# Kernel tuning notes

Hardware: AMD Instinct MI355X
Metric: run time of the kernel (lower is better)

The kernel has to match this reference:

```python
import jax, jax.numpy as jnp
import numpy as np

B, S, H = 32, 256, 128
K, C, DSUB, O = 8, 4096, 16, 6  # PQ subspaces, ncentroids=4096, subvector dim, bits/symbol


def setup_inputs() -> dict:
    key = jax.random.key(0)
    ks = jax.random.split(key, 8)
    return {
        "z": jax.random.normal(ks[0], (B, S, 3), jnp.float32),
        "W1": jax.random.normal(ks[1], (3, H), jnp.float32) * 0.3,
        "b1": jax.random.normal(ks[2], (H,), jnp.float32) * 0.1,
        "W2": jax.random.normal(ks[3], (H, H), jnp.float32) * 0.1,
        "b2": jax.random.normal(ks[4], (H,), jnp.float32) * 0.1,
        "centroids": jax.random.normal(ks[5], (K, C, DSUB), jnp.float32),
        "W3": jax.random.normal(ks[6], (H, O), jnp.float32) * 0.1,
        "b3": jax.random.normal(ks[7], (O,), jnp.float32) * 0.1,
    }


def reference(z, W1, b1, W2, b2, centroids, W3, b3):
    # Small demapper MLP (layers 1-2, exact dense math)
    h1 = jax.nn.relu(z @ W1 + b1)            # [B,S,H]
    h2 = jax.nn.relu(h1 @ W2 + b2)           # [B,S,H] == layer3in
    N = B * S
    x = h2.reshape(N, K, DSUB)               # split rows into K PQ subvectors
    # Encode: nearest centroid per subspace (||x-c||^2 argmin; ||x||^2 is constant per row)
    dots = jnp.einsum("nkd,kcd->nkc", x, centroids)      # [N,K,C]
    c_norm = jnp.sum(centroids * centroids, axis=-1)      # [K,C]
    codes = jnp.argmin(c_norm[None, :, :] - 2.0 * dots, axis=-1)  # [N,K] int
    # LUT: precomputed centroid @ W3 per subspace
    W3r = W3.reshape(K, DSUB, O)
    lut = jnp.einsum("kcd,kdo->kco", centroids, W3r)      # [K,C,O]
    # Approximate matmul: sum of LUT entries selected by codes
    approx = jnp.sum(lut[jnp.arange(K)[None, :], codes], axis=1)  # [N,O]
    llr = (approx + b3).reshape(B, S * O)                 # [B, n]
    return llr
```

## Files before the change

kernel.cpp:

```cpp
#include <hip/hip_runtime.h>
#include <hip/hip_fp16.h>
#include <stdint.h>

#define NROWS 8192
#define HDIM  128
#define KSUB  8
#define NC    4096
#define DSUB  16
#define OUTD  6

#define FB_TAU 3e-4f
#define DOTSCALE (-2.0f / 4096.0f)

typedef _Float16 f16x8 __attribute__((ext_vector_type(8)));
typedef float    f32x4 __attribute__((ext_vector_type(4)));

#define XK_OFF 0u
#define CN_OFF 4194304u
#define B1_OFF 4325376u
#define PK_OFF 6422528u

__global__ __launch_bounds__(256) void prep_kernel(
    const float* __restrict__ z, const float* __restrict__ W1, const float* __restrict__ b1,
    const float* __restrict__ W2, const float* __restrict__ b2,
    const float* __restrict__ ce,
    float* __restrict__ xk, float* __restrict__ cnorm, f16x8* __restrict__ B1S)
{
    __shared__ float h1s[32 * HDIM];
    __shared__ float w2s[HDIM * HDIM];
    const int t = threadIdx.x;
    const int row0 = blockIdx.x * 32;

    #pragma unroll
    for (int q = 0; q < 2; ++q) {
        const int e = blockIdx.x * 512 + q * 256 + t;
        const int k    = e >> 14;
        const int tile = (e >> 6) & 255;
        const int lane = e & 63;
        const int col  = lane & 15;
        const int quad = lane >> 4;
        const int dims = (quad & 1) * 8;
        const int part = quad >> 1;
        const int n = tile * 16 + col;
        const float* cp = &ce[((size_t)k * NC + n) * DSUB + dims];
        f16x8 hi, lo;
        #pragma unroll
        for (int j = 0; j < 8; ++j) {
            const float s = cp[j] * 16.0f;
            const _Float16 h = (_Float16)s;
            hi[j] = h;
            lo[j] = (_Float16)(s - (float)h);
        }
        B1S[e] = part ? lo : hi;
    }

    if (blockIdx.x < (KSUB * NC) / 256) {
        const int g = blockIdx.x * 256 + t;
        const float4* cp = (const float4*)&ce[(size_t)g * DSUB];
        float nn = 0.f;
        #pragma unroll
        for (int q = 0; q < 4; ++q) {
            const float4 v = cp[q];
            nn = fmaf(v.x, v.x, nn); nn = fmaf(v.y, v.y, nn);
            nn = fmaf(v.z, v.z, nn); nn = fmaf(v.w, v.w, nn);
        }
        cnorm[g] = nn;
    }

    {
        const float4* g4 = (const float4*)W2;
        float4* s4 = (float4*)w2s;
        #pragma unroll
        for (int q = 0; q < 16; ++q) s4[t + q * 256] = g4[t + q * 256];
    }

    #pragma unroll
    for (int e = 0; e < 16; ++e) {
        const int idx = e * 256 + t;
        const int r = idx >> 7, j = idx & 127;
        const int n = row0 + r;
        float acc = b1[j];
        acc = fmaf(z[n * 3 + 0], W1[0 * HDIM + j], acc);
        acc = fmaf(z[n * 3 + 1], W1[1 * HDIM + j], acc);
        acc = fmaf(z[n * 3 + 2], W1[2 * HDIM + j], acc);
        h1s[idx] = fmaxf(acc, 0.f);
    }
    __syncthreads();

    const int c4 = (t & 31) * 4;
    const int r4 = (t >> 5) * 4;
    float acc[4][4];
    #pragma unroll
    for (int a = 0; a < 4; ++a)
        #pragma unroll
        for (int b = 0; b < 4; ++b) acc[a][b] = 0.f;

    for (int k4 = 0; k4 < HDIM; k4 += 4) {
        float hh[4][4], ww[4][4];
        #pragma unroll
        for (int q = 0; q < 4; ++q) {
            const float4 v = *(const float4*)&h1s[(r4 + q) * HDIM + k4];
            hh[q][0] = v.x; hh[q][1] = v.y; hh[q][2] = v.z; hh[q][3] = v.w;
        }
        #pragma unroll
        for (int p = 0; p < 4; ++p) {
            const float4 v = *(const float4*)&w2s[(k4 + p) * HDIM + c4];
            ww[p][0] = v.x; ww[p][1] = v.y; ww[p][2] = v.z; ww[p][3] = v.w;
        }
        #pragma unroll
        for (int q = 0; q < 4; ++q)
            #pragma unroll
            for (int p = 0; p < 4; ++p) {
                acc[q][0] = fmaf(hh[q][p], ww[p][0], acc[q][0]);
                acc[q][1] = fmaf(hh[q][p], ww[p][1], acc[q][1]);
                acc[q][2] = fmaf(hh[q][p], ww[p][2], acc[q][2]);
                acc[q][3] = fmaf(hh[q][p], ww[p][3], acc[q][3]);
            }
    }

    const float4 bb = *(const float4*)&b2[c4];
    const int kk = c4 >> 4;
    const int dd = c4 & 15;
    #pragma unroll
    for (int q = 0; q < 4; ++q) {
        float4 o;
        o.x = fmaxf(acc[q][0] + bb.x, 0.f);
        o.y = fmaxf(acc[q][1] + bb.y, 0.f);
        o.z = fmaxf(acc[q][2] + bb.z, 0.f);
        o.w = fmaxf(acc[q][3] + bb.w, 0.f);
        *(float4*)&xk[((size_t)kk * NROWS + (row0 + r4 + q)) * DSUB + dd] = o;
    }
}

__global__ __launch_bounds__(256, 4) void argmin_kernel(
    const float* __restrict__ xk, const f16x8* __restrict__ B1S,
    const float* __restrict__ cnorm, unsigned long long* __restrict__ pk)
{
    __shared__ f16x8 cs[16 * 64];
    __shared__ float cnL[1024];
    const int t = threadIdx.x;
    const int lane = t & 63;
    const int wid  = t >> 6;
    const int k  = blockIdx.y;
    const int cz = blockIdx.z;
    const int rb = blockIdx.x * 4 + wid;
    const int col  = lane & 15;
    const int quad = lane >> 4;
    const int dims = (quad & 1) * 8;
    const int part = quad >> 1;

    {
        const float* cnp0 = &cnorm[k * NC + cz * 1024];
        #pragma unroll
        for (int q = 0; q < 4; ++q) cnL[t + q * 256] = cnp0[t + q * 256];
    }

    f16x8 A[2];
    #pragma unroll
    for (int g = 0; g < 2; ++g) {
        const int row = rb * 32 + g * 16 + col;
        const float* xp = &xk[((size_t)k * NROWS + row) * DSUB + dims];
        f16x8 hi, lo;
        #pragma unroll
        for (int j = 0; j < 8; ++j) {
            const float s = xp[j] * 256.0f;
            const _Float16 h = (_Float16)s;
            hi[j] = h;
            lo[j] = (_Float16)(s - (float)h);
        }
        A[g] = part ? lo : hi;
    }

    float m1[2][4], m2[2][4];
    int   idx[2][4];
    #pragma unroll
    for (int g = 0; g < 2; ++g)
        #pragma unroll
        for (int j = 0; j < 4; ++j) { m1[g][j] = 1e30f; m2[g][j] = 1e30f; idx[g][j] = 0; }

    const f16x8* gp = &B1S[((size_t)k * 256 + cz * 64) * 64];

    for (int ch = 0; ch < 4; ++ch) {
        __syncthreads();
        {
            const uint4* g4 = (const uint4*)(gp + (size_t)ch * 1024);
            uint4* s4 = (uint4*)cs;
            #pragma unroll
            for (int q = 0; q < 4; ++q) s4[t + q * 256] = g4[t + q * 256];
        }
        __syncthreads();

        #pragma unroll 2
        for (int tt = 0; tt < 16; ++tt) {
            const f16x8 b1 = cs[tt * 64 + lane];
            const f16x8 b2 = cs[tt * 64 + (lane ^ 32)];
            const float nrm = cnL[(ch * 16 + tt) * 16 + col];
            const f32x4 zz = {0.f, 0.f, 0.f, 0.f};
            f32x4 p0 = __builtin_amdgcn_mfma_f32_16x16x32_f16(A[0], b1, zz, 0, 0, 0);
            p0       = __builtin_amdgcn_mfma_f32_16x16x32_f16(A[0], b2, p0, 0, 0, 0);
            f32x4 p1 = __builtin_amdgcn_mfma_f32_16x16x32_f16(A[1], b1, zz, 0, 0, 0);
            p1       = __builtin_amdgcn_mfma_f32_16x16x32_f16(A[1], b2, p1, 0, 0, 0);
            const int c = ((cz * 64 + ch * 16 + tt) << 4) + col;
            #pragma unroll
            for (int j = 0; j < 4; ++j) {
                {
                    const float s = fmaf(p0[j], DOTSCALE, nrm);
                    const bool lt = s < m1[0][j];
                    m2[0][j] = __builtin_amdgcn_fmed3f(s, m1[0][j], m2[0][j]);
                    idx[0][j] = lt ? c : idx[0][j];
                    m1[0][j] = fminf(s, m1[0][j]);
                }
                {
                    const float s = fmaf(p1[j], DOTSCALE, nrm);
                    const bool lt = s < m1[1][j];
                    m2[1][j] = __builtin_amdgcn_fmed3f(s, m1[1][j], m2[1][j]);
                    idx[1][j] = lt ? c : idx[1][j];
                    m1[1][j] = fminf(s, m1[1][j]);
                }
            }
        }
    }

    #pragma unroll
    for (int off = 1; off < 16; off <<= 1) {
        #pragma unroll
        for (int g = 0; g < 2; ++g)
            #pragma unroll
            for (int j = 0; j < 4; ++j) {
                const float om1 = __shfl_xor(m1[g][j], off, 64);
                const float om2 = __shfl_xor(m2[g][j], off, 64);
                const int  oidx = __shfl_xor(idx[g][j], off, 64);
                const bool better = (om1 < m1[g][j]) ||
                                    (om1 == m1[g][j] && oidx < idx[g][j]);
                m2[g][j] = fminf(fminf(m2[g][j], om2), fmaxf(m1[g][j], om1));
                m1[g][j] = better ? om1 : m1[g][j];
                idx[g][j] = better ? oidx : idx[g][j];
            }
    }

    if (col == 0) {
        #pragma unroll
        for (int g = 0; g < 2; ++g)
            #pragma unroll
            for (int j = 0; j < 4; ++j) {
                const int row = rb * 32 + g * 16 + quad * 4 + j;
                unsigned u = __float_as_uint(m1[g][j]);
                u = (u & 0x80000000u) ? ~u : (u | 0x80000000u);
                const unsigned short dh =
                    __half_as_ushort(__float2half(m2[g][j] - m1[g][j]));
                pk[((size_t)cz * NROWS + row) * KSUB + k] =
                    ((unsigned long long)u << 32) |
                    ((unsigned)dh << 16) | (unsigned)idx[g][j];
            }
    }
}

__global__ __launch_bounds__(256) void finish_kernel(
    const float* __restrict__ xk, const float* __restrict__ ce,
    const float* __restrict__ cnorm, const unsigned long long* __restrict__ pk,
    const float* __restrict__ W3, const float* __restrict__ b3,
    float* __restrict__ out)
{
    __shared__ int codes_s[256];
    __shared__ int wl_s[256];
    __shared__ int wcnt;
    const int t = threadIdx.x;
    const int row0 = blockIdx.x * 32;
    if (t == 0) wcnt = 0;
    __syncthreads();

    {
        const int row = row0 + (t >> 3);
        const int k = t & 7;
        unsigned long long p[4];
        #pragma unroll
        for (int s = 0; s < 4; ++s)
            p[s] = pk[((size_t)s * NROWS + row) * KSUB + k];
        unsigned long long w = p[0];
        #pragma unroll
        for (int s = 1; s < 4; ++s) w = p[s] < w ? p[s] : w;
        const unsigned uw = (unsigned)(w >> 32);
        const float m1w = __uint_as_float((uw & 0x80000000u) ? (uw ^ 0x80000000u) : ~uw);
        float m2g = m1w + (float)__ushort_as_half((unsigned short)((unsigned)w >> 16));
        #pragma unroll
        for (int s = 0; s < 4; ++s) {
            if (p[s] != w) {
                const unsigned us = (unsigned)(p[s] >> 32);
                m2g = fminf(m2g, __uint_as_float(
                    (us & 0x80000000u) ? (us ^ 0x80000000u) : ~us));
            }
        }
        codes_s[t] = (int)(w & 0xFFFFull);
        if (m2g - m1w < FB_TAU) {
            const int slot = atomicAdd(&wcnt, 1);
            wl_s[slot] = t;
        }
    }
    __syncthreads();

    {
        const int lane = t & 63;
        const int wid = t >> 6;
        const int nitems = wcnt;
        for (int i = wid; i < nitems; i += 4) {
            const int wg = wl_s[i];
            const int row = row0 + (wg >> 3), k = wg & 7;
            float xr[DSUB];
            {
                const float* xp = &xk[((size_t)k * NROWS + row) * DSUB];
                #pragma unroll
                for (int q = 0; q < DSUB; q += 4) {
                    const float4 v = *(const float4*)&xp[q];
                    xr[q + 0] = -2.f * v.x; xr[q + 1] = -2.f * v.y;
                    xr[q + 2] = -2.f * v.z; xr[q + 3] = -2.f * v.w;
                }
            }
            float bm = 1e30f; int bi = NC;
            for (int c = lane; c < NC; c += 64) {
                const float* cp = &ce[((size_t)k * NC + c) * DSUB];
                float s = cnorm[k * NC + c];
                #pragma unroll
                for (int d = 0; d < DSUB; ++d) s = fmaf(xr[d], cp[d], s);
                if (s < bm) { bm = s; bi = c; }
            }
            #pragma unroll
            for (int off = 1; off < 64; off <<= 1) {
                const float om = __shfl_xor(bm, off, 64);
                const int  oi = __shfl_xor(bi, off, 64);
                const bool better = (om < bm) || (om == bm && oi < bi);
                bm = better ? om : bm;
                bi = better ? oi : bi;
            }
            if (lane == 0) codes_s[wg] = bi;
        }
    }
    __syncthreads();

    if (t < 32 * OUTD) {
        const int nl = t / OUTD;
        const int o = t - nl * OUTD;
        const int n = row0 + nl;
        float acc = b3[o];
        #pragma unroll
        for (int k = 0; k < KSUB; ++k) {
            const int code = codes_s[nl * KSUB + k];
            const float* cp = &ce[((size_t)k * NC + code) * DSUB];
            const float* wp = &W3[(k * DSUB) * OUTD + o];
            #pragma unroll
            for (int d = 0; d < DSUB; ++d)
                acc = fmaf(cp[d], wp[d * OUTD], acc);
        }
        out[n * OUTD + o] = acc;
    }
}

extern "C" void kernel_launch(void* const* d_in, const int* in_sizes, int n_in,
                              void* d_out, int out_size, void* d_ws, size_t ws_size,
                              hipStream_t stream)
{
    const float* z  = (const float*)d_in[0];
    const float* W1 = (const float*)d_in[1];
    const float* b1 = (const float*)d_in[2];
    const float* W2 = (const float*)d_in[3];
    const float* b2 = (const float*)d_in[4];
    const float* ce = (const float*)d_in[5];
    const float* W3 = (const float*)d_in[6];
    const float* b3 = (const float*)d_in[7];

    char* ws = (char*)d_ws;
    float* xk    = (float*)(ws + XK_OFF);
    float* cnorm = (float*)(ws + CN_OFF);
    f16x8* B1S   = (f16x8*)(ws + B1_OFF);
    unsigned long long* pk = (unsigned long long*)(ws + PK_OFF);

    hipLaunchKernelGGL(prep_kernel, dim3(256), dim3(256), 0, stream,
                       z, W1, b1, W2, b2, ce, xk, cnorm, B1S);
    hipLaunchKernelGGL(argmin_kernel, dim3(64, 8, 4), dim3(256), 0, stream,
                       xk, B1S, cnorm, pk);
    hipLaunchKernelGGL(finish_kernel, dim3(256), dim3(256), 0, stream,
                       xk, ce, cnorm, pk, W3, b3, (float*)d_out);
}
```

Measured before the change: 170.4 us.

## Switch argmin to 32x32x16 MFMA tiles and halve centroid splits

Replaces the 16x16x32 MFMA tiling in the argmin kernel with 32x32x16 MFMA. Each wave handles 32 rows by 32 centroids per step, with the hi/lo fp16 split now carried as four explicit MFMAs. The centroid split dimension drops from 4 to 2, so each block covers 2048 centroids with twice the LDS staging, and finish merges only two partial results. The aim is fewer LDS reads per MFMA and larger outputs per instruction, at the cost of more accumulator registers (16 rows of m1, m2 and idx) and half as many blocks in the grid.

```diff
diff --git a/kernel.cpp b/kernel.cpp
--- a/kernel.cpp
+++ b/kernel.cpp
@@ -13,18 +13,18 @@
 #define DOTSCALE (-2.0f / 4096.0f)
 
 typedef _Float16 f16x8 __attribute__((ext_vector_type(8)));
-typedef float    f32x4 __attribute__((ext_vector_type(4)));
+typedef float    f32x16 __attribute__((ext_vector_type(16)));
 
 #define XK_OFF 0u
 #define CN_OFF 4194304u
-#define B1_OFF 4325376u
+#define B2_OFF 4325376u
 #define PK_OFF 6422528u
 
 __global__ __launch_bounds__(256) void prep_kernel(
     const float* __restrict__ z, const float* __restrict__ W1, const float* __restrict__ b1,
     const float* __restrict__ W2, const float* __restrict__ b2,
     const float* __restrict__ ce,
-    float* __restrict__ xk, float* __restrict__ cnorm, f16x8* __restrict__ B1S)
+    float* __restrict__ xk, float* __restrict__ cnorm, f16x8* __restrict__ B2S)
 {
     __shared__ float h1s[32 * HDIM];
     __shared__ float w2s[HDIM * HDIM];
@@ -35,13 +35,11 @@
     for (int q = 0; q < 2; ++q) {
         const int e = blockIdx.x * 512 + q * 256 + t;
         const int k    = e >> 14;
-        const int tile = (e >> 6) & 255;
+        const int unit = (e >> 7) & 127;
+        const int half = (e >> 6) & 1;
         const int lane = e & 63;
-        const int col  = lane & 15;
-        const int quad = lane >> 4;
-        const int dims = (quad & 1) * 8;
-        const int part = quad >> 1;
-        const int n = tile * 16 + col;
+        const int n    = unit * 32 + (lane & 31);
+        const int dims = (lane >> 5) * 8;
         const float* cp = &ce[((size_t)k * NC + n) * DSUB + dims];
         f16x8 hi, lo;
         #pragma unroll
@@ -51,7 +49,7 @@
             hi[j] = h;
             lo[j] = (_Float16)(s - (float)h);
         }
-        B1S[e] = part ? lo : hi;
+        B2S[e] = half ? lo : hi;
     }
 
     if (blockIdx.x < (KSUB * NC) / 256) {
@@ -133,125 +131,105 @@
 }
 
 __global__ __launch_bounds__(256, 4) void argmin_kernel(
-    const float* __restrict__ xk, const f16x8* __restrict__ B1S,
+    const float* __restrict__ xk, const f16x8* __restrict__ B2S,
     const float* __restrict__ cnorm, unsigned long long* __restrict__ pk)
 {
-    __shared__ f16x8 cs[16 * 64];
-    __shared__ float cnL[1024];
+    __shared__ f16x8 cs[16 * 2 * 64];
+    __shared__ float cnS[2048];
     const int t = threadIdx.x;
     const int lane = t & 63;
     const int wid  = t >> 6;
     const int k  = blockIdx.y;
     const int cz = blockIdx.z;
-    const int rb = blockIdx.x * 4 + wid;
-    const int col  = lane & 15;
-    const int quad = lane >> 4;
-    const int dims = (quad & 1) * 8;
-    const int part = quad >> 1;
-
-    {
-        const float* cnp0 = &cnorm[k * NC + cz * 1024];
-        #pragma unroll
-        for (int q = 0; q < 4; ++q) cnL[t + q * 256] = cnp0[t + q * 256];
-    }
-
-    f16x8 A[2];
-    #pragma unroll
-    for (int g = 0; g < 2; ++g) {
-        const int row = rb * 32 + g * 16 + col;
-        const float* xp = &xk[((size_t)k * NROWS + row) * DSUB + dims];
-        f16x8 hi, lo;
+    const int rowbase = blockIdx.x * 128 + wid * 32;
+    const int col = lane & 31;
+    const int khl = lane >> 5;
+
+    {
+        const float* cnp0 = &cnorm[k * NC + cz * 2048];
+        #pragma unroll
+        for (int q = 0; q < 8; ++q) cnS[t + q * 256] = cnp0[t + q * 256];
+    }
+
+    f16x8 Ah, Al;
+    {
+        const float* xp = &xk[((size_t)k * NROWS + rowbase + col) * DSUB + khl * 8];
         #pragma unroll
         for (int j = 0; j < 8; ++j) {
             const float s = xp[j] * 256.0f;
             const _Float16 h = (_Float16)s;
-            hi[j] = h;
-            lo[j] = (_Float16)(s - (float)h);
-        }
-        A[g] = part ? lo : hi;
-    }
-
-    float m1[2][4], m2[2][4];
-    int   idx[2][4];
-    #pragma unroll
-    for (int g = 0; g < 2; ++g)
-        #pragma unroll
-        for (int j = 0; j < 4; ++j) { m1[g][j] = 1e30f; m2[g][j] = 1e30f; idx[g][j] = 0; }
-
-    const f16x8* gp = &B1S[((size_t)k * 256 + cz * 64) * 64];
+            Ah[j] = h;
+            Al[j] = (_Float16)(s - (float)h);
+        }
+    }
+
+    float m1[16], m2[16];
+    int   idx[16];
+    #pragma unroll
+    for (int r = 0; r < 16; ++r) { m1[r] = 1e30f; m2[r] = 1e30f; idx[r] = 0; }
+
+    const f16x8* gB = &B2S[((size_t)(k * 128 + cz * 64)) * 128];
+    const f32x16 zero16 = {0.f,0.f,0.f,0.f,0.f,0.f,0.f,0.f,
+                           0.f,0.f,0.f,0.f,0.f,0.f,0.f,0.f};
 
     for (int ch = 0; ch < 4; ++ch) {
         __syncthreads();
         {
-            const uint4* g4 = (const uint4*)(gp + (size_t)ch * 1024);
+            const uint4* g4 = (const uint4*)gB + ch * 2048;
             uint4* s4 = (uint4*)cs;
             #pragma unroll
-            for (int q = 0; q < 4; ++q) s4[t + q * 256] = g4[t + q * 256];
+            for (int q = 0; q < 8; ++q) s4[t + q * 256] = g4[t + q * 256];
         }
         __syncthreads();
 
         #pragma unroll 2
-        for (int tt = 0; tt < 16; ++tt) {
-            const f16x8 b1 = cs[tt * 64 + lane];
-            const f16x8 b2 = cs[tt * 64 + (lane ^ 32)];
-            const float nrm = cnL[(ch * 16 + tt) * 16 + col];
-            const f32x4 zz = {0.f, 0.f, 0.f, 0.f};
-            f32x4 p0 = __builtin_amdgcn_mfma_f32_16x16x32_f16(A[0], b1, zz, 0, 0, 0);
-            p0       = __builtin_amdgcn_mfma_f32_16x16x32_f16(A[0], b2, p0, 0, 0, 0);
-            f32x4 p1 = __builtin_amdgcn_mfma_f32_16x16x32_f16(A[1], b1, zz, 0, 0, 0);
-            p1       = __builtin_amdgcn_mfma_f32_16x16x32_f16(A[1], b2, p1, 0, 0, 0);
-            const int c = ((cz * 64 + ch * 16 + tt) << 4) + col;
-            #pragma unroll
-            for (int j = 0; j < 4; ++j) {
-                {
-                    const float s = fmaf(p0[j], DOTSCALE, nrm);
-                    const bool lt = s < m1[0][j];
-                    m2[0][j] = __builtin_amdgcn_fmed3f(s, m1[0][j], m2[0][j]);
-                    idx[0][j] = lt ? c : idx[0][j];
-                    m1[0][j] = fminf(s, m1[0][j]);
-                }
-                {
-                    const float s = fmaf(p1[j], DOTSCALE, nrm);
-                    const bool lt = s < m1[1][j];
-                    m2[1][j] = __builtin_amdgcn_fmed3f(s, m1[1][j], m2[1][j]);
-                    idx[1][j] = lt ? c : idx[1][j];
-                    m1[1][j] = fminf(s, m1[1][j]);
-                }
-            }
-        }
-    }
-
-    #pragma unroll
-    for (int off = 1; off < 16; off <<= 1) {
-        #pragma unroll
-        for (int g = 0; g < 2; ++g)
-            #pragma unroll
-            for (int j = 0; j < 4; ++j) {
-                const float om1 = __shfl_xor(m1[g][j], off, 64);
-                const float om2 = __shfl_xor(m2[g][j], off, 64);
-                const int  oidx = __shfl_xor(idx[g][j], off, 64);
-                const bool better = (om1 < m1[g][j]) ||
-                                    (om1 == m1[g][j] && oidx < idx[g][j]);
-                m2[g][j] = fminf(fminf(m2[g][j], om2), fmaxf(m1[g][j], om1));
-                m1[g][j] = better ? om1 : m1[g][j];
-                idx[g][j] = better ? oidx : idx[g][j];
-            }
+        for (int u = 0; u < 16; ++u) {
+            const f16x8 Bh = cs[u * 128 + lane];
+            const f16x8 Bl = cs[u * 128 + 64 + lane];
+            const float nrm = cnS[(ch * 16 + u) * 32 + col];
+            f32x16 acc = __builtin_amdgcn_mfma_f32_32x32x16_f16(Ah, Bh, zero16, 0, 0, 0);
+            acc = __builtin_amdgcn_mfma_f32_32x32x16_f16(Al, Bl, acc, 0, 0, 0);
+            acc = __builtin_amdgcn_mfma_f32_32x32x16_f16(Ah, Bl, acc, 0, 0, 0);
+            acc = __builtin_amdgcn_mfma_f32_32x32x16_f16(Al, Bh, acc, 0, 0, 0);
+            const int c = cz * 2048 + (ch * 16 + u) * 32 + col;
+            #pragma unroll
+            for (int r = 0; r < 16; ++r) {
+                const float s = fmaf(acc[r], DOTSCALE, nrm);
+                const bool lt = s < m1[r];
+                m2[r] = __builtin_amdgcn_fmed3f(s, m1[r], m2[r]);
+                idx[r] = lt ? c : idx[r];
+                m1[r] = fminf(s, m1[r]);
+            }
+        }
+    }
+
+    #pragma unroll
+    for (int off = 1; off < 32; off <<= 1) {
+        #pragma unroll
+        for (int r = 0; r < 16; ++r) {
+            const float om1 = __shfl_xor(m1[r], off, 64);
+            const float om2 = __shfl_xor(m2[r], off, 64);
+            const int  oidx = __shfl_xor(idx[r], off, 64);
+            const bool better = (om1 < m1[r]) ||
+                                (om1 == m1[r] && oidx < idx[r]);
+            m2[r] = fminf(fminf(m2[r], om2), fmaxf(m1[r], om1));
+            m1[r] = better ? om1 : m1[r];
+            idx[r] = better ? oidx : idx[r];
+        }
     }
 
     if (col == 0) {
         #pragma unroll
-        for (int g = 0; g < 2; ++g)
-            #pragma unroll
-            for (int j = 0; j < 4; ++j) {
-                const int row = rb * 32 + g * 16 + quad * 4 + j;
-                unsigned u = __float_as_uint(m1[g][j]);
-                u = (u & 0x80000000u) ? ~u : (u | 0x80000000u);
-                const unsigned short dh =
-                    __half_as_ushort(__float2half(m2[g][j] - m1[g][j]));
-                pk[((size_t)cz * NROWS + row) * KSUB + k] =
-                    ((unsigned long long)u << 32) |
-                    ((unsigned)dh << 16) | (unsigned)idx[g][j];
-            }
+        for (int r = 0; r < 16; ++r) {
+            const int row = rowbase + (r & 3) + 8 * (r >> 2) + 4 * khl;
+            unsigned u = __float_as_uint(m1[r]);
+            u = (u & 0x80000000u) ? ~u : (u | 0x80000000u);
+            const unsigned short dh =
+                __half_as_ushort(__float2half(m2[r] - m1[r]));
+            pk[((size_t)cz * NROWS + row) * KSUB + k] =
+                ((unsigned long long)u << 32) |
+                ((unsigned)dh << 16) | (unsigned)idx[r];
+        }
     }
 }
 
@@ -272,24 +250,15 @@
     {
         const int row = row0 + (t >> 3);
         const int k = t & 7;
-        unsigned long long p[4];
-        #pragma unroll
-        for (int s = 0; s < 4; ++s)
-            p[s] = pk[((size_t)s * NROWS + row) * KSUB + k];
-        unsigned long long w = p[0];
-        #pragma unroll
-        for (int s = 1; s < 4; ++s) w = p[s] < w ? p[s] : w;
-        const unsigned uw = (unsigned)(w >> 32);
+        const unsigned long long a = pk[(size_t)row * KSUB + k];
+        const unsigned long long b = pk[((size_t)NROWS + row) * KSUB + k];
+        const unsigned long long w = a < b ? a : b;
+        const unsigned long long l = a < b ? b : a;
+        const unsigned uw = (unsigned)(w >> 32), ul = (unsigned)(l >> 32);
         const float m1w = __uint_as_float((uw & 0x80000000u) ? (uw ^ 0x80000000u) : ~uw);
-        float m2g = m1w + (float)__ushort_as_half((unsigned short)((unsigned)w >> 16));
-        #pragma unroll
-        for (int s = 0; s < 4; ++s) {
-            if (p[s] != w) {
-                const unsigned us = (unsigned)(p[s] >> 32);
-                m2g = fminf(m2g, __uint_as_float(
-                    (us & 0x80000000u) ? (us ^ 0x80000000u) : ~us));
-            }
-        }
+        const float m1l = __uint_as_float((ul & 0x80000000u) ? (ul ^ 0x80000000u) : ~ul);
+        const float m2g = fminf(
+            m1w + (float)__ushort_as_half((unsigned short)((unsigned)w >> 16)), m1l);
         codes_s[t] = (int)(w & 0xFFFFull);
         if (m2g - m1w < FB_TAU) {
             const int slot = atomicAdd(&wcnt, 1);
@@ -370,13 +339,13 @@
     char* ws = (char*)d_ws;
     float* xk    = (float*)(ws + XK_OFF);
     float* cnorm = (float*)(ws + CN_OFF);
-    f16x8* B1S   = (f16x8*)(ws + B1_OFF);
+    f16x8* B2S   = (f16x8*)(ws + B2_OFF);
     unsigned long long* pk = (unsigned long long*)(ws + PK_OFF);
 
     hipLaunchKernelGGL(prep_kernel, dim3(256), dim3(256), 0, stream,
-                       z, W1, b1, W2, b2, ce, xk, cnorm, B1S);
-    hipLaunchKernelGGL(argmin_kernel, dim3(64, 8, 4), dim3(256), 0, stream,
-                       xk, B1S, cnorm, pk);
+                       z, W1, b1, W2, b2, ce, xk, cnorm, B2S);
+    hipLaunchKernelGGL(argmin_kernel, dim3(64, 8, 2), dim3(256), 0, stream,
+                       xk, B2S, cnorm, pk);
     hipLaunchKernelGGL(finish_kernel, dim3(256), dim3(256), 0, stream,
                        xk, ce, cnorm, pk, W3, b3, (float*)d_out);
 }
```

Result: slower. 174.9 us (+2.6%).
